# Kernel tuning notes

Measured on AMD Instinct MI355X. Metric: run time of the kernel, lower is better.

The kernel has to match this reference:

```python
import jax, jax.numpy as jnp
import numpy as np


def setup_inputs() -> dict:
    key = jax.random.key(0)
    ks = jax.random.split(key, 7)
    B, C, H, W = 16, 256, 1, 4096
    x = jax.random.normal(ks[0], (B, C, H, W), dtype=jnp.float32)
    init = lambda k, s: jax.random.normal(k, s, dtype=jnp.float32) * 0.02
    return {
        "x": x,
        "Wq": init(ks[1], (C, C)), "bq": jnp.zeros((C,), jnp.float32),
        "Wk": init(ks[2], (C, C)), "bk": jnp.zeros((C,), jnp.float32),
        "Wv": init(ks[3], (C, C)), "bv": jnp.zeros((C,), jnp.float32),
    }


def reference(x, Wq, bq, Wk, bk, Wv, bv):
    B, C, H, W = x.shape
    xs = jnp.transpose(x[:, :, 0, :], (0, 2, 1))  # [B, W, C]
    Q = xs @ Wq.T + bq  # [B, W, C]
    K = xs @ Wk.T + bk
    V = xs @ Wv.T + bv
    scale = jnp.sqrt(jnp.asarray(C, dtype=Q.dtype))

    # radius-1 sliding window along width; pad so window gather is static
    Kp = jnp.pad(K, ((0, 0), (1, 1), (0, 0)))  # [B, W+2, C]
    Vp = jnp.pad(V, ((0, 0), (1, 1), (0, 0)))
    idx = jnp.arange(W)[:, None] + jnp.arange(3)[None, :]  # padded indices [W,3]
    pos = idx - 1  # original positions (may be -1 or W -> invalid at edges)
    valid = (pos >= 0) & (pos < W)  # [W, 3]

    Kw = Kp[:, idx]  # [B, W, 3, C]
    Vw = Vp[:, idx]  # [B, W, 3, C]

    scores = jnp.einsum('bwc,bwkc->bwk', Q, Kw) / scale  # [B, W, 3]
    scores = jnp.where(valid[None], scores, jnp.asarray(-1e9, scores.dtype))
    attn = jax.nn.softmax(scores, axis=-1)
    out = jnp.einsum('bwk,bwkc->bwc', attn, Vw)  # [B, W, C]
    # [B, W, C] -> [B, C, 1, W]
    return jnp.transpose(out, (0, 2, 1))[:, :, None, :]
```

## Files before the change

### kernel.cpp

```cpp
#include <hip/hip_runtime.h>
#include <hip/hip_bf16.h>

#define C_DIM 256
#define W_DIM 4096
#define WI 62
#define NCH 67
#define LDS_BYTES 49664

typedef unsigned short u16;
typedef short s16x8 __attribute__((ext_vector_type(8)));
typedef unsigned short u16x8 __attribute__((ext_vector_type(8)));
typedef unsigned short u16x4 __attribute__((ext_vector_type(4)));
typedef float f32x16 __attribute__((ext_vector_type(16)));

__device__ __forceinline__ u16 f2b(float f) {
  return __builtin_bit_cast(u16, __float2bfloat16(f));
}
__device__ __forceinline__ float b2f(u16 u) {
  return __builtin_bit_cast(float, ((unsigned)u) << 16);
}

__global__ __launch_bounds__(256) void prep_kernel(
    const float* __restrict__ Wq, const float* __restrict__ bq,
    const float* __restrict__ Wk, const float* __restrict__ bk,
    const float* __restrict__ Wv, char* __restrict__ ws) {
  u16* Mb   = (u16*)ws;
  u16* Wvb  = (u16*)(ws + 131072);
  float* u0 = (float*)(ws + 262144);
  float* u1 = (float*)(ws + 263168);
  float* c0p = (float*)(ws + 264192);
  int bid = blockIdx.x, t = threadIdx.x;
  if (bid < 256) {
    __shared__ float Wqs[256*17];
    __shared__ float Wks[256*17];
    int i0 = (bid >> 4) << 4, j0 = (bid & 15) << 4;
    for (int it = 0; it < 16; ++it) {
      int e = t + 256*it; int a = e >> 4, ii = e & 15;
      Wqs[a*17+ii] = Wq[a*256 + i0 + ii];
      Wks[a*17+ii] = Wk[a*256 + j0 + ii];
    }
    __syncthreads();
    int ii = t >> 4, jj = t & 15;
    float acc = 0.f;
    #pragma unroll 8
    for (int a = 0; a < 256; ++a) acc += Wqs[a*17+ii] * Wks[a*17+jj];
    Mb[(i0+ii)*256 + j0 + jj] = f2b(acc);
  } else if (bid == 256) {
    int j = t;
    float a0 = 0.f, a1 = 0.f;
    #pragma unroll 4
    for (int a = 0; a < 256; ++a) {
      a0 += bq[a] * Wk[a*256 + j];
      a1 += bk[a] * Wq[a*256 + j];
    }
    u0[j] = a0; u1[j] = a1;
    __shared__ float red[256];
    red[t] = bq[t] * bk[t];
    __syncthreads();
    if (t == 0) { float s = 0.f; for (int a = 0; a < 256; ++a) s += red[a]; *c0p = s; }
  } else {
    int base = ((bid - 257)*256 + t) * 4;
    const float4 v = *reinterpret_cast<const float4*>(Wv + base);
    ushort4 pk = make_ushort4(f2b(v.x), f2b(v.y), f2b(v.z), f2b(v.w));
    *reinterpret_cast<ushort4*>(Wvb + base) = pk;
  }
}

__global__ __launch_bounds__(512, 6) void main_kernel(
    const float* __restrict__ x, const char* __restrict__ ws,
    const float* __restrict__ bv, float* __restrict__ out) {
  const u16* Mb   = (const u16*)ws;
  const u16* Wvb  = (const u16*)(ws + 131072);
  const float* u0 = (const float*)(ws + 262144);
  const float* u1 = (const float*)(ws + 263168);
  const float c0  = *(const float*)(ws + 264192);

  extern __shared__ char lds[];
  u16* Xt    = (u16*)lds;
  float* PsA = (float*)(lds + 32768);
  float* PsB = (float*)(lds + 36864);
  float* ABs = (float*)(lds + 49152);

  const int bid = blockIdx.x;
  const int b = bid / NCH, cw = bid % NCH;
  const int w0 = cw * WI;
  const int t = threadIdx.x;
  const int wv = t >> 6, l = t & 63;
  const int col = l & 31, half = l >> 5;

  {
    const float* xb = x + (size_t)b * (C_DIM * W_DIM);
    int wg = w0 - 1 + l;
    bool ok = (wg >= 0) & (wg < W_DIM);
    const float* xp = xb + wg;
    float xr[32];
    #pragma unroll
    for (int it = 0; it < 4; ++it)
      #pragma unroll
      for (int e = 0; e < 8; ++e) {
        int c = (wv + 8*it)*8 + e;
        xr[it*8+e] = ok ? xp[(size_t)c * W_DIM] : 0.f;
      }
    float pa = 0.f, pb = 0.f;
    #pragma unroll
    for (int it = 0; it < 4; ++it) {
      int kk = wv + 8*it;
      union { u16 u[8]; u16x8 v; } pk;
      #pragma unroll
      for (int e = 0; e < 8; ++e) {
        float v = xr[it*8+e];
        pk.u[e] = f2b(v);
        int c = kk*8 + e;
        pa += u0[c] * v;
        pb += u1[c] * v;
      }
      *reinterpret_cast<u16x8*>(Xt + (kk*64 + l)*8) = pk.v;
    }
    PsA[wv*64 + l] = pa;
    PsA[512 + wv*64 + l] = pb;
  }
  __syncthreads();

  f32x16 acc0, acc1;
  #pragma unroll
  for (int r = 0; r < 16; ++r) { acc0[r] = 0.f; acc1[r] = 0.f; }
  {
    const u16* Arow = Mb + (32*wv + col)*256 + 8*half;
    #pragma unroll
    for (int kk = 0; kk < 16; ++kk) {
      s16x8 a = *reinterpret_cast<const s16x8*>(Arow + 16*kk);
      int kx = 2*kk + half;
      s16x8 b0 = *reinterpret_cast<const s16x8*>(Xt + (kx*64 + col)*8);
      s16x8 b1 = *reinterpret_cast<const s16x8*>(Xt + (kx*64 + col + 32)*8);
      acc0 = __builtin_amdgcn_mfma_f32_32x32x16_bf16(a, b0, acc0, 0, 0, 0);
      acc1 = __builtin_amdgcn_mfma_f32_32x32x16_bf16(a, b1, acc1, 0, 0, 0);
    }
  }
  if (t < 128) {
    int u = t & 63, which = t >> 6;
    float s = 0.f;
    #pragma unroll
    for (int g = 0; g < 8; ++g) s += PsA[which*512 + g*64 + u];
    ABs[which*64 + u] = s;
  }

  {
    float s0a=0.f, s1a=0.f, s2a=0.f, s0b=0.f, s1b=0.f, s2b=0.f;
    const int e0 = 4*half;
    const int wmm = (col > 0)  ? col-1  : 0;
    const int wpp = (col < 31) ? col+33 : 63;
    #pragma unroll
    for (int q = 0; q < 4; ++q) {
      const u16* base = Xt + (4*wv + q)*64*8 + e0;
      u16x4 xm0 = *reinterpret_cast<const u16x4*>(base + wmm*8);
      u16x4 xc0 = *reinterpret_cast<const u16x4*>(base + col*8);
      u16x4 xp0 = *reinterpret_cast<const u16x4*>(base + (col+1)*8);
      u16x4 xm1 = *reinterpret_cast<const u16x4*>(base + (col+31)*8);
      u16x4 xc1 = *reinterpret_cast<const u16x4*>(base + (col+32)*8);
      u16x4 xp1 = *reinterpret_cast<const u16x4*>(base + wpp*8);
      #pragma unroll
      for (int r4 = 0; r4 < 4; ++r4) {
        float g0 = acc0[4*q + r4], g1 = acc1[4*q + r4];
        s2a += g0 * b2f(xm0[r4]);
        s1a += g0 * b2f(xc0[r4]);
        s0a += g0 * b2f(xp0[r4]);
        s2b += g1 * b2f(xm1[r4]);
        s1b += g1 * b2f(xc1[r4]);
        s0b += g1 * b2f(xp1[r4]);
      }
    }
    float* PB = PsB + (wv*2 + half)*64;
    PB[0*1024 + col+1] = s0a;
    if (col < 31) PB[0*1024 + col+33] = s0b;
    PB[1*1024 + col]    = s1a;
    PB[1*1024 + col+32] = s1b;
    if (col > 0) PB[2*1024 + col-1] = s2a;
    PB[2*1024 + col+31] = s2b;
  }
  __syncthreads();

  {
    float a0 = 0.f, a1 = 0.f, a2 = 0.f;
    const bool interior = (l >= 1) && (l <= WI);
    if (interior) {
      float d0 = 0.f, d1 = 0.f, d2 = 0.f;
      #pragma unroll
      for (int g = 0; g < 16; ++g) {
        d0 += PsB[g*64 + l];
        d1 += PsB[1024 + g*64 + l];
        d2 += PsB[2048 + g*64 + l];
      }
      int wgc = w0 - 1 + l;
      float alm = ABs[l-1], alc = ABs[l], alp = ABs[l+1], be = ABs[64+l];
      float sc0 = (d0 + alm + be + c0) * 0.0625f;
      float sc1 = (d1 + alc + be + c0) * 0.0625f;
      float sc2 = (d2 + alp + be + c0) * 0.0625f;
      bool v0 = (wgc - 1 >= 0);
      bool v1 = (wgc < W_DIM);
      bool v2 = (wgc + 1 < W_DIM);
      if (v1) {
        const float NEG = -1e30f;
        float m = fmaxf(v0 ? sc0 : NEG, fmaxf(sc1, v2 ? sc2 : NEG));
        float e0 = v0 ? __expf(sc0 - m) : 0.f;
        float e1 = __expf(sc1 - m);
        float e2 = v2 ? __expf(sc2 - m) : 0.f;
        float inv = 1.f / (e0 + e1 + e2);
        a0 = e0*inv; a1 = e1*inv; a2 = e2*inv;
      }
    }
    u16x8 xmix[4];
    #pragma unroll
    for (int kg = 0; kg < 4; ++kg) {
      const u16* base = Xt + (4*wv + kg)*64*8;
      u16x8 xm = *reinterpret_cast<const u16x8*>(base + (l > 0  ? l-1 : 0 )*8);
      u16x8 xc = *reinterpret_cast<const u16x8*>(base + l*8);
      u16x8 xp = *reinterpret_cast<const u16x8*>(base + (l < 63 ? l+1 : 63)*8);
      union { u16 u[8]; u16x8 v; } pk;
      #pragma unroll
      for (int e = 0; e < 8; ++e)
        pk.u[e] = f2b(a0*b2f(xm[e]) + a1*b2f(xc[e]) + a2*b2f(xp[e]));
      xmix[kg] = pk.v;
    }
    if (interior) {
      #pragma unroll
      for (int kg = 0; kg < 4; ++kg)
        *reinterpret_cast<u16x8*>(Xt + ((4*wv + kg)*64 + l)*8) = xmix[kg];
    }
  }
  __syncthreads();

  {
    #pragma unroll
    for (int r = 0; r < 16; ++r) { acc0[r] = 0.f; acc1[r] = 0.f; }
    float bvr[16];
    #pragma unroll
    for (int q = 0; q < 4; ++q) {
      float4 t4 = *reinterpret_cast<const float4*>(bv + 32*wv + 8*q + 4*half);
      bvr[4*q+0] = t4.x; bvr[4*q+1] = t4.y; bvr[4*q+2] = t4.z; bvr[4*q+3] = t4.w;
    }
    const u16* Arow = Wvb + (32*wv + col)*256 + 8*half;
    #pragma unroll
    for (int kk = 0; kk < 16; ++kk) {
      s16x8 a = *reinterpret_cast<const s16x8*>(Arow + 16*kk);
      int kx = 2*kk + half;
      s16x8 b0 = *reinterpret_cast<const s16x8*>(Xt + (kx*64 + col)*8);
      s16x8 b1 = *reinterpret_cast<const s16x8*>(Xt + (kx*64 + col + 32)*8);
      acc0 = __builtin_amdgcn_mfma_f32_32x32x16_bf16(a, b0, acc0, 0, 0, 0);
      acc1 = __builtin_amdgcn_mfma_f32_32x32x16_bf16(a, b1, acc1, 0, 0, 0);
    }
    float* outb = out + (size_t)b * (C_DIM * W_DIM);
    int wg0 = w0 - 1 + col, wg1 = wg0 + 32;
    bool st0 = (col >= 1) && (wg0 < W_DIM);
    bool st1 = (col <= 30) && (wg1 < W_DIM);
    #pragma unroll
    for (int r = 0; r < 16; ++r) {
      int crow = 32*wv + (r&3) + 8*(r>>2) + 4*half;
      if (st0) outb[(size_t)crow*W_DIM + wg0] = acc0[r] + bvr[r];
      if (st1) outb[(size_t)crow*W_DIM + wg1] = acc1[r] + bvr[r];
    }
  }
}

extern "C" void kernel_launch(void* const* d_in, const int* in_sizes, int n_in,
                              void* d_out, int out_size, void* d_ws, size_t ws_size,
                              hipStream_t stream) {
  (void)in_sizes; (void)n_in; (void)out_size; (void)ws_size;
  const float* x  = (const float*)d_in[0];
  const float* Wq = (const float*)d_in[1];
  const float* bq = (const float*)d_in[2];
  const float* Wk = (const float*)d_in[3];
  const float* bk = (const float*)d_in[4];
  const float* Wv = (const float*)d_in[5];
  const float* bv = (const float*)d_in[6];
  float* out = (float*)d_out;
  char* ws = (char*)d_ws;

  hipFuncSetAttribute((const void*)main_kernel,
                      hipFuncAttributeMaxDynamicSharedMemorySize, LDS_BYTES);
  prep_kernel<<<321, 256, 0, stream>>>(Wq, bq, Wk, bk, Wv, ws);
  main_kernel<<<16 * NCH, 512, LDS_BYTES, stream>>>(x, ws, bv, out);
}
```

Baseline: 93.09 us.

## Process two 64-wide tiles per block with double-buffered prefetch of next tile

Each block now handles two adjacent 64-column tiles, using 66-column halo buffers so every output column is computed once instead of recomputing overlap halos across 62-wide chunks. While the first tile runs its QK-fold MFMAs, softmax and V projection, the next tile's x slices are loaded into registers and written to a second LDS buffer in stages. The score path uses a third MFMA accumulator for the halo columns and a wave shuffle reduction in place of the larger partial-sum buffer. LDS per block grows to about 77 KB, so occupancy drops (launch bounds 512,4) and the grid shrinks to 512 blocks.

```diff
diff --git a/kernel.cpp b/kernel.cpp
--- a/kernel.cpp
+++ b/kernel.cpp
@@ -3,9 +3,7 @@
 
 #define C_DIM 256
 #define W_DIM 4096
-#define WI 62
-#define NCH 67
-#define LDS_BYTES 49664
+#define LDS_BYTES 78672
 
 typedef unsigned short u16;
 typedef short s16x8 __attribute__((ext_vector_type(8)));
@@ -66,7 +64,7 @@
   }
 }
 
-__global__ __launch_bounds__(512, 6) void main_kernel(
+__global__ __launch_bounds__(512, 4) void main_kernel(
     const float* __restrict__ x, const char* __restrict__ ws,
     const float* __restrict__ bv, float* __restrict__ out) {
   const u16* Mb   = (const u16*)ws;
@@ -76,188 +74,297 @@
   const float c0  = *(const float*)(ws + 264192);
 
   extern __shared__ char lds[];
-  u16* Xt    = (u16*)lds;
-  float* PsA = (float*)(lds + 32768);
-  float* PsB = (float*)(lds + 36864);
-  float* ABs = (float*)(lds + 49152);
+  u16* Xa    = (u16*)lds;
+  float* PsA = (float*)(lds + 67584);
+  float* PsB = (float*)(lds + 71808);
+  float* ABs = (float*)(lds + 78144);
 
   const int bid = blockIdx.x;
-  const int b = bid / NCH, cw = bid % NCH;
-  const int w0 = cw * WI;
   const int t = threadIdx.x;
   const int wv = t >> 6, l = t & 63;
   const int col = l & 31, half = l >> 5;
 
+  const int gi0 = 2*bid;
+  const int b   = gi0 >> 6;
+  const int cw0 = gi0 & 63;
+  const float* xb = x + (size_t)b * (C_DIM*W_DIM);
+  float* outb = out + (size_t)b * (C_DIM*W_DIM);
+
   {
-    const float* xb = x + (size_t)b * (C_DIM * W_DIM);
+    const int w0 = cw0 * 64;
     int wg = w0 - 1 + l;
-    bool ok = (wg >= 0) & (wg < W_DIM);
+    bool ok = (wg >= 0);
     const float* xp = xb + wg;
-    float xr[32];
     #pragma unroll
-    for (int it = 0; it < 4; ++it)
-      #pragma unroll
-      for (int e = 0; e < 8; ++e) {
-        int c = (wv + 8*it)*8 + e;
-        xr[it*8+e] = ok ? xp[(size_t)c * W_DIM] : 0.f;
-      }
-    float pa = 0.f, pb = 0.f;
-    #pragma unroll
-    for (int it = 0; it < 4; ++it) {
-      int kk = wv + 8*it;
-      union { u16 u[8]; u16x8 v; } pk;
-      #pragma unroll
-      for (int e = 0; e < 8; ++e) {
-        float v = xr[it*8+e];
-        pk.u[e] = f2b(v);
-        int c = kk*8 + e;
-        pa += u0[c] * v;
-        pb += u1[c] * v;
-      }
-      *reinterpret_cast<u16x8*>(Xt + (kk*64 + l)*8) = pk.v;
-    }
-    PsA[wv*64 + l] = pa;
-    PsA[512 + wv*64 + l] = pb;
+    for (int r = 0; r < 4; ++r) {
+      int kk = wv + 8*r;
+      float v[8];
+      #pragma unroll
+      for (int e = 0; e < 8; ++e)
+        v[e] = ok ? xp[(size_t)(kk*8+e) * W_DIM] : 0.f;
+      union { u16 u[8]; u16x8 vv; } pk;
+      #pragma unroll
+      for (int e = 0; e < 8; ++e) pk.u[e] = f2b(v[e]);
+      *reinterpret_cast<u16x8*>(Xa + (kk*66 + l)*8) = pk.vv;
+    }
+    if (t < 64) {
+      int j = 64 + (t & 1), kk = t >> 1;
+      int wge = w0 - 1 + j;
+      bool oke = (wge < W_DIM);
+      const float* xpe = xb + wge;
+      union { u16 u[8]; u16x8 vv; } pk;
+      #pragma unroll
+      for (int e = 0; e < 8; ++e)
+        pk.u[e] = oke ? f2b(xpe[(size_t)(kk*8+e)*W_DIM]) : (u16)0;
+      *reinterpret_cast<u16x8*>(Xa + (kk*66 + j)*8) = pk.vv;
+    }
   }
   __syncthreads();
 
-  f32x16 acc0, acc1;
   #pragma unroll
-  for (int r = 0; r < 16; ++r) { acc0[r] = 0.f; acc1[r] = 0.f; }
-  {
+  for (int i = 0; i < 2; ++i) {
+    const bool pf = (i == 0);
+    u16* Xc = Xa + (i ? 16896 : 0);
+    u16* Xn = Xa + (i ? 0 : 16896);
+    const int cw = cw0 + i;
+    const int w0 = cw * 64;
+    const int w0n = w0 + 64;
+
+    float pfv[8], pfe[8];
+    const float* xpn = xb + (w0n - 1 + l);
+
+    if (pf) {
+      #pragma unroll
+      for (int e = 0; e < 8; ++e) pfv[e] = xpn[(size_t)(wv*8+e)*W_DIM];
+      if (t < 64) {
+        int j = 64 + (t&1), kk = t>>1;
+        bool oke = (w0n - 1 + j) < W_DIM;
+        const float* xpe = xb + (w0n - 1 + j);
+        #pragma unroll
+        for (int e = 0; e < 8; ++e) pfe[e] = oke ? xpe[(size_t)(kk*8+e)*W_DIM] : 0.f;
+      }
+    }
+
+    f32x16 acc0, acc1, acc2;
+    #pragma unroll
+    for (int r = 0; r < 16; ++r) { acc0[r] = 0.f; acc1[r] = 0.f; acc2[r] = 0.f; }
     const u16* Arow = Mb + (32*wv + col)*256 + 8*half;
     #pragma unroll
-    for (int kk = 0; kk < 16; ++kk) {
+    for (int kk = 0; kk < 8; ++kk) {
       s16x8 a = *reinterpret_cast<const s16x8*>(Arow + 16*kk);
-      int kx = 2*kk + half;
-      s16x8 b0 = *reinterpret_cast<const s16x8*>(Xt + (kx*64 + col)*8);
-      s16x8 b1 = *reinterpret_cast<const s16x8*>(Xt + (kx*64 + col + 32)*8);
+      const u16* Bb = Xc + (2*kk + half)*66*8;
+      s16x8 b0 = *reinterpret_cast<const s16x8*>(Bb + col*8);
+      s16x8 b1 = *reinterpret_cast<const s16x8*>(Bb + (col+32)*8);
+      s16x8 b2 = *reinterpret_cast<const s16x8*>(Bb + (col+64)*8);
       acc0 = __builtin_amdgcn_mfma_f32_32x32x16_bf16(a, b0, acc0, 0, 0, 0);
       acc1 = __builtin_amdgcn_mfma_f32_32x32x16_bf16(a, b1, acc1, 0, 0, 0);
-    }
-  }
-  if (t < 128) {
-    int u = t & 63, which = t >> 6;
-    float s = 0.f;
+      acc2 = __builtin_amdgcn_mfma_f32_32x32x16_bf16(a, b2, acc2, 0, 0, 0);
+    }
+    if (pf) {
+      union { u16 u[8]; u16x8 vv; } pk;
+      #pragma unroll
+      for (int e = 0; e < 8; ++e) pk.u[e] = f2b(pfv[e]);
+      *reinterpret_cast<u16x8*>(Xn + (wv*66 + l)*8) = pk.vv;
+      #pragma unroll
+      for (int e = 0; e < 8; ++e) pfv[e] = xpn[(size_t)((wv+8)*8+e)*W_DIM];
+    }
     #pragma unroll
-    for (int g = 0; g < 8; ++g) s += PsA[which*512 + g*64 + u];
-    ABs[which*64 + u] = s;
-  }
-
-  {
-    float s0a=0.f, s1a=0.f, s2a=0.f, s0b=0.f, s1b=0.f, s2b=0.f;
-    const int e0 = 4*half;
-    const int wmm = (col > 0)  ? col-1  : 0;
-    const int wpp = (col < 31) ? col+33 : 63;
-    #pragma unroll
-    for (int q = 0; q < 4; ++q) {
-      const u16* base = Xt + (4*wv + q)*64*8 + e0;
-      u16x4 xm0 = *reinterpret_cast<const u16x4*>(base + wmm*8);
-      u16x4 xc0 = *reinterpret_cast<const u16x4*>(base + col*8);
-      u16x4 xp0 = *reinterpret_cast<const u16x4*>(base + (col+1)*8);
-      u16x4 xm1 = *reinterpret_cast<const u16x4*>(base + (col+31)*8);
-      u16x4 xc1 = *reinterpret_cast<const u16x4*>(base + (col+32)*8);
-      u16x4 xp1 = *reinterpret_cast<const u16x4*>(base + wpp*8);
-      #pragma unroll
-      for (int r4 = 0; r4 < 4; ++r4) {
-        float g0 = acc0[4*q + r4], g1 = acc1[4*q + r4];
-        s2a += g0 * b2f(xm0[r4]);
-        s1a += g0 * b2f(xc0[r4]);
-        s0a += g0 * b2f(xp0[r4]);
-        s2b += g1 * b2f(xm1[r4]);
-        s1b += g1 * b2f(xc1[r4]);
-        s0b += g1 * b2f(xp1[r4]);
-      }
-    }
-    float* PB = PsB + (wv*2 + half)*64;
-    PB[0*1024 + col+1] = s0a;
-    if (col < 31) PB[0*1024 + col+33] = s0b;
-    PB[1*1024 + col]    = s1a;
-    PB[1*1024 + col+32] = s1b;
-    if (col > 0) PB[2*1024 + col-1] = s2a;
-    PB[2*1024 + col+31] = s2b;
-  }
-  __syncthreads();
-
-  {
-    float a0 = 0.f, a1 = 0.f, a2 = 0.f;
-    const bool interior = (l >= 1) && (l <= WI);
-    if (interior) {
-      float d0 = 0.f, d1 = 0.f, d2 = 0.f;
-      #pragma unroll
-      for (int g = 0; g < 16; ++g) {
-        d0 += PsB[g*64 + l];
-        d1 += PsB[1024 + g*64 + l];
-        d2 += PsB[2048 + g*64 + l];
-      }
-      int wgc = w0 - 1 + l;
-      float alm = ABs[l-1], alc = ABs[l], alp = ABs[l+1], be = ABs[64+l];
-      float sc0 = (d0 + alm + be + c0) * 0.0625f;
-      float sc1 = (d1 + alc + be + c0) * 0.0625f;
-      float sc2 = (d2 + alp + be + c0) * 0.0625f;
-      bool v0 = (wgc - 1 >= 0);
-      bool v1 = (wgc < W_DIM);
-      bool v2 = (wgc + 1 < W_DIM);
-      if (v1) {
-        const float NEG = -1e30f;
-        float m = fmaxf(v0 ? sc0 : NEG, fmaxf(sc1, v2 ? sc2 : NEG));
-        float e0 = v0 ? __expf(sc0 - m) : 0.f;
-        float e1 = __expf(sc1 - m);
-        float e2 = v2 ? __expf(sc2 - m) : 0.f;
-        float inv = 1.f / (e0 + e1 + e2);
-        a0 = e0*inv; a1 = e1*inv; a2 = e2*inv;
-      }
-    }
-    u16x8 xmix[4];
-    #pragma unroll
-    for (int kg = 0; kg < 4; ++kg) {
-      const u16* base = Xt + (4*wv + kg)*64*8;
-      u16x8 xm = *reinterpret_cast<const u16x8*>(base + (l > 0  ? l-1 : 0 )*8);
-      u16x8 xc = *reinterpret_cast<const u16x8*>(base + l*8);
-      u16x8 xp = *reinterpret_cast<const u16x8*>(base + (l < 63 ? l+1 : 63)*8);
-      union { u16 u[8]; u16x8 v; } pk;
-      #pragma unroll
-      for (int e = 0; e < 8; ++e)
-        pk.u[e] = f2b(a0*b2f(xm[e]) + a1*b2f(xc[e]) + a2*b2f(xp[e]));
-      xmix[kg] = pk.v;
-    }
-    if (interior) {
-      #pragma unroll
-      for (int kg = 0; kg < 4; ++kg)
-        *reinterpret_cast<u16x8*>(Xt + ((4*wv + kg)*64 + l)*8) = xmix[kg];
-    }
-  }
-  __syncthreads();
-
-  {
-    #pragma unroll
-    for (int r = 0; r < 16; ++r) { acc0[r] = 0.f; acc1[r] = 0.f; }
-    float bvr[16];
-    #pragma unroll
-    for (int q = 0; q < 4; ++q) {
-      float4 t4 = *reinterpret_cast<const float4*>(bv + 32*wv + 8*q + 4*half);
-      bvr[4*q+0] = t4.x; bvr[4*q+1] = t4.y; bvr[4*q+2] = t4.z; bvr[4*q+3] = t4.w;
-    }
-    const u16* Arow = Wvb + (32*wv + col)*256 + 8*half;
-    #pragma unroll
-    for (int kk = 0; kk < 16; ++kk) {
+    for (int kk = 8; kk < 16; ++kk) {
       s16x8 a = *reinterpret_cast<const s16x8*>(Arow + 16*kk);
-      int kx = 2*kk + half;
-      s16x8 b0 = *reinterpret_cast<const s16x8*>(Xt + (kx*64 + col)*8);
-      s16x8 b1 = *reinterpret_cast<const s16x8*>(Xt + (kx*64 + col + 32)*8);
+      const u16* Bb = Xc + (2*kk + half)*66*8;
+      s16x8 b0 = *reinterpret_cast<const s16x8*>(Bb + col*8);
+      s16x8 b1 = *reinterpret_cast<const s16x8*>(Bb + (col+32)*8);
+      s16x8 b2 = *reinterpret_cast<const s16x8*>(Bb + (col+64)*8);
       acc0 = __builtin_amdgcn_mfma_f32_32x32x16_bf16(a, b0, acc0, 0, 0, 0);
       acc1 = __builtin_amdgcn_mfma_f32_32x32x16_bf16(a, b1, acc1, 0, 0, 0);
-    }
-    float* outb = out + (size_t)b * (C_DIM * W_DIM);
-    int wg0 = w0 - 1 + col, wg1 = wg0 + 32;
-    bool st0 = (col >= 1) && (wg0 < W_DIM);
-    bool st1 = (col <= 30) && (wg1 < W_DIM);
-    #pragma unroll
-    for (int r = 0; r < 16; ++r) {
-      int crow = 32*wv + (r&3) + 8*(r>>2) + 4*half;
-      if (st0) outb[(size_t)crow*W_DIM + wg0] = acc0[r] + bvr[r];
-      if (st1) outb[(size_t)crow*W_DIM + wg1] = acc1[r] + bvr[r];
-    }
+      acc2 = __builtin_amdgcn_mfma_f32_32x32x16_bf16(a, b2, acc2, 0, 0, 0);
+    }
+    if (pf) {
+      union { u16 u[8]; u16x8 vv; } pk;
+      #pragma unroll
+      for (int e = 0; e < 8; ++e) pk.u[e] = f2b(pfv[e]);
+      *reinterpret_cast<u16x8*>(Xn + ((wv+8)*66 + l)*8) = pk.vv;
+      #pragma unroll
+      for (int e = 0; e < 8; ++e) pfv[e] = xpn[(size_t)((wv+16)*8+e)*W_DIM];
+    }
+
+    {
+      float pa = 0.f, pb_ = 0.f;
+      #pragma unroll
+      for (int kg = 0; kg < 4; ++kg) {
+        int kk = 4*wv + kg;
+        u16x8 xv = *reinterpret_cast<const u16x8*>(Xc + (kk*66 + l)*8);
+        #pragma unroll
+        for (int e = 0; e < 8; ++e) {
+          float xf = b2f(xv[e]);
+          pa  += u0[kk*8+e] * xf;
+          pb_ += u1[kk*8+e] * xf;
+        }
+      }
+      PsA[wv*66 + l] = pa;
+      PsA[528 + wv*66 + l] = pb_;
+      if (l < 2) {
+        float ea = 0.f, eb = 0.f;
+        #pragma unroll
+        for (int kg = 0; kg < 4; ++kg) {
+          int kk = 4*wv + kg;
+          u16x8 xv = *reinterpret_cast<const u16x8*>(Xc + (kk*66 + 64 + l)*8);
+          #pragma unroll
+          for (int e = 0; e < 8; ++e) {
+            float xf = b2f(xv[e]);
+            ea += u0[kk*8+e] * xf;
+            eb += u1[kk*8+e] * xf;
+          }
+        }
+        PsA[wv*66 + 64 + l] = ea;
+        PsA[528 + wv*66 + 64 + l] = eb;
+      }
+    }
+    __syncthreads();
+
+    if (pf) {
+      union { u16 u[8]; u16x8 vv; } pk;
+      #pragma unroll
+      for (int e = 0; e < 8; ++e) pk.u[e] = f2b(pfv[e]);
+      *reinterpret_cast<u16x8*>(Xn + ((wv+16)*66 + l)*8) = pk.vv;
+      #pragma unroll
+      for (int e = 0; e < 8; ++e) pfv[e] = xpn[(size_t)((wv+24)*8+e)*W_DIM];
+    }
+    if (t < 132) {
+      int which = (t >= 66) ? 1 : 0, jj = t - 66*which;
+      float s = 0.f;
+      #pragma unroll
+      for (int g = 0; g < 8; ++g) s += PsA[which*528 + g*66 + jj];
+      ABs[which*66 + jj] = s;
+    }
+    {
+      float t0s0=0.f,t0s1=0.f,t0s2=0.f,t1s0=0.f,t1s1=0.f,t1s2=0.f,t2s1=0.f,t2s2=0.f;
+      const int e0 = 4*half;
+      int jm0 = (col > 0) ? col-1 : 0;
+      int jm2 = (63+col > 65) ? 65 : 63+col;
+      int jc2 = (64+col > 65) ? 65 : 64+col;
+      #pragma unroll
+      for (int q = 0; q < 4; ++q) {
+        const u16* base = Xc + (4*wv + q)*66*8 + e0;
+        u16x4 xT0m = *reinterpret_cast<const u16x4*>(base + jm0*8);
+        u16x4 xT0c = *reinterpret_cast<const u16x4*>(base + col*8);
+        u16x4 xT0p = *reinterpret_cast<const u16x4*>(base + (col+1)*8);
+        u16x4 xT1m = *reinterpret_cast<const u16x4*>(base + (col+31)*8);
+        u16x4 xT1c = *reinterpret_cast<const u16x4*>(base + (col+32)*8);
+        u16x4 xT1p = *reinterpret_cast<const u16x4*>(base + (col+33)*8);
+        u16x4 xT2m = *reinterpret_cast<const u16x4*>(base + jm2*8);
+        u16x4 xT2c = *reinterpret_cast<const u16x4*>(base + jc2*8);
+        #pragma unroll
+        for (int r4 = 0; r4 < 4; ++r4) {
+          float g0 = acc0[4*q+r4], g1 = acc1[4*q+r4], g2 = acc2[4*q+r4];
+          t0s1 += g0 * b2f(xT0c[r4]);
+          t0s0 += g0 * b2f(xT0p[r4]);
+          t0s2 += g0 * b2f(xT0m[r4]);
+          t1s1 += g1 * b2f(xT1c[r4]);
+          t1s0 += g1 * b2f(xT1p[r4]);
+          t1s2 += g1 * b2f(xT1m[r4]);
+          t2s1 += g2 * b2f(xT2c[r4]);
+          t2s2 += g2 * b2f(xT2m[r4]);
+        }
+      }
+      t0s0 += __shfl_xor(t0s0, 32); t0s1 += __shfl_xor(t0s1, 32);
+      t0s2 += __shfl_xor(t0s2, 32); t1s0 += __shfl_xor(t1s0, 32);
+      t1s1 += __shfl_xor(t1s1, 32); t1s2 += __shfl_xor(t1s2, 32);
+      t2s1 += __shfl_xor(t2s1, 32); t2s2 += __shfl_xor(t2s2, 32);
+      float* PBw = PsB + wv*66;
+      if (half == 0) {
+        PBw[0*528 + col+1]  = t0s0;
+        PBw[1*528 + col]    = t0s1;
+        if (col >= 1) PBw[2*528 + col-1] = t0s2;
+        PBw[0*528 + col+33] = t1s0;
+        PBw[1*528 + col+32] = t1s1;
+        PBw[2*528 + col+31] = t1s2;
+      } else if (col < 2) {
+        PBw[1*528 + col+64] = t2s1;
+        PBw[2*528 + col+63] = t2s2;
+      }
+    }
+    __syncthreads();
+
+    if (pf) {
+      union { u16 u[8]; u16x8 vv; } pk;
+      #pragma unroll
+      for (int e = 0; e < 8; ++e) pk.u[e] = f2b(pfv[e]);
+      *reinterpret_cast<u16x8*>(Xn + ((wv+24)*66 + l)*8) = pk.vv;
+      if (t < 64) {
+        int j = 64 + (t&1), kk = t>>1;
+        union { u16 u[8]; u16x8 vv; } pke;
+        #pragma unroll
+        for (int e = 0; e < 8; ++e) pke.u[e] = f2b(pfe[e]);
+        *reinterpret_cast<u16x8*>(Xn + (kk*66 + j)*8) = pke.vv;
+      }
+    }
+
+    {
+      float d0 = 0.f, d1 = 0.f, d2 = 0.f;
+      #pragma unroll
+      for (int g = 0; g < 8; ++g) {
+        d0 += PsB[0*528 + g*66 + l+1];
+        d1 += PsB[1*528 + g*66 + l+1];
+        d2 += PsB[2*528 + g*66 + l+1];
+      }
+      float am = ABs[l], ac = ABs[l+1], ap = ABs[l+2];
+      float be = ABs[66 + l+1];
+      float sc0 = (d0 + am + be + c0) * 0.0625f;
+      float sc1 = (d1 + ac + be + c0) * 0.0625f;
+      float sc2 = (d2 + ap + be + c0) * 0.0625f;
+      int w = w0 + l;
+      bool v0 = (w >= 1), v2 = (w + 1 < W_DIM);
+      const float NEG = -1e30f;
+      float m = fmaxf(v0 ? sc0 : NEG, fmaxf(sc1, v2 ? sc2 : NEG));
+      float e0v = v0 ? __expf(sc0 - m) : 0.f;
+      float e1v = __expf(sc1 - m);
+      float e2v = v2 ? __expf(sc2 - m) : 0.f;
+      float inv = 1.f / (e0v + e1v + e2v);
+      float a0 = e0v*inv, a1 = e1v*inv, a2 = e2v*inv;
+      #pragma unroll
+      for (int kg = 0; kg < 4; ++kg) {
+        int kk = 4*wv + kg;
+        const u16* base = Xc + kk*66*8;
+        u16x8 xm = *reinterpret_cast<const u16x8*>(base + l*8);
+        u16x8 xc_ = *reinterpret_cast<const u16x8*>(base + (l+1)*8);
+        u16x8 xp = *reinterpret_cast<const u16x8*>(base + (l+2)*8);
+        union { u16 u[8]; u16x8 vv; } pk;
+        #pragma unroll
+        for (int e = 0; e < 8; ++e)
+          pk.u[e] = f2b(a0*b2f(xm[e]) + a1*b2f(xc_[e]) + a2*b2f(xp[e]));
+        *reinterpret_cast<u16x8*>(const_cast<u16*>(base) + (l+1)*8) = pk.vv;
+      }
+    }
+    __syncthreads();
+
+    {
+      #pragma unroll
+      for (int r = 0; r < 16; ++r) { acc0[r] = 0.f; acc1[r] = 0.f; }
+      const u16* Arow2 = Wvb + (32*wv + col)*256 + 8*half;
+      #pragma unroll
+      for (int kk = 0; kk < 16; ++kk) {
+        s16x8 a = *reinterpret_cast<const s16x8*>(Arow2 + 16*kk);
+        const u16* Bb = Xc + (2*kk + half)*66*8;
+        s16x8 b0 = *reinterpret_cast<const s16x8*>(Bb + (1+col)*8);
+        s16x8 b1 = *reinterpret_cast<const s16x8*>(Bb + (33+col)*8);
+        acc0 = __builtin_amdgcn_mfma_f32_32x32x16_bf16(a, b0, acc0, 0, 0, 0);
+        acc1 = __builtin_amdgcn_mfma_f32_32x32x16_bf16(a, b1, acc1, 0, 0, 0);
+      }
+      float bvr[16];
+      #pragma unroll
+      for (int q = 0; q < 4; ++q) {
+        float4 t4 = *reinterpret_cast<const float4*>(bv + 32*wv + 8*q + 4*half);
+        bvr[4*q+0] = t4.x; bvr[4*q+1] = t4.y; bvr[4*q+2] = t4.z; bvr[4*q+3] = t4.w;
+      }
+      #pragma unroll
+      for (int r = 0; r < 16; ++r) {
+        int crow = 32*wv + (r&3) + 8*(r>>2) + 4*half;
+        outb[(size_t)crow*W_DIM + w0 + col]      = acc0[r] + bvr[r];
+        outb[(size_t)crow*W_DIM + w0 + 32 + col] = acc1[r] + bvr[r];
+      }
+    }
+    __syncthreads();
   }
 }
 
@@ -278,5 +385,5 @@
   hipFuncSetAttribute((const void*)main_kernel,
                       hipFuncAttributeMaxDynamicSharedMemorySize, LDS_BYTES);
   prep_kernel<<<321, 256, 0, stream>>>(Wq, bq, Wk, bk, Wv, ws);
-  main_kernel<<<16 * NCH, 512, LDS_BYTES, stream>>>(x, ws, bv, out);
-}
+  main_kernel<<<512, 512, LDS_BYTES, stream>>>(x, ws, bv, out);
+}
```

After: 99.36 us. 1.07x slower.
